# Performance work log

Measured on AMD Instinct MI355X. Metric: run time of the kernel, lower is better.

## Reference

```python
import jax, jax.numpy as jnp
import numpy as np

K = 15  # dynamic kernel size (out conv emits 15*15=225 channels)


def conv3x3(x, w, b):
    # x: [B,C,H,W], w: [O,I,3,3] (OIHW), 'SAME' padding, stride 1
    y = jax.lax.conv_general_dilated(
        x, w, window_strides=(1, 1), padding='SAME',
        dimension_numbers=('NCHW', 'OIHW', 'NCHW'))
    return y + b[None, :, None, None]


def res_block(x, wa, ba, wb, bb):
    # ResidualBlock_noBN: x + conv(relu(conv(x)))
    return x + conv3x3(jax.nn.relu(conv3x3(x, wa, ba)), wb, bb)


def setup_inputs() -> dict:
    key = jax.random.key(0)
    ks = jax.random.split(key, 12)
    nf = 64

    def w(k, o, i):
        return jax.random.normal(k, (o, i, 3, 3), jnp.float32) * 0.05

    return {
        'data_with_est': jax.random.normal(ks[0], (4, 6, 256, 256), jnp.float32),
        'data': jax.random.normal(ks[1], (4, 3, 256, 256), jnp.float32),
        'w_first': w(ks[2], nf, 6), 'b_first': jnp.zeros((nf,), jnp.float32),
        'w1a': w(ks[3], nf, nf), 'b1a': jnp.zeros((nf,), jnp.float32),
        'w1b': w(ks[4], nf, nf), 'b1b': jnp.zeros((nf,), jnp.float32),
        'w2a': w(ks[5], nf, nf), 'b2a': jnp.zeros((nf,), jnp.float32),
        'w2b': w(ks[6], nf, nf), 'b2b': jnp.zeros((nf,), jnp.float32),
        'w3a': w(ks[7], nf, nf), 'b3a': jnp.zeros((nf,), jnp.float32),
        'w3b': w(ks[8], nf, nf), 'b3b': jnp.zeros((nf,), jnp.float32),
        'w_out': w(ks[9], K * K, nf), 'b_out': jnp.zeros((K * K,), jnp.float32),
    }


def kernel_conv(frames, core):
    # frames: [B,3,H,W]; core: [B,225,H,W]
    B, C, H, W = frames.shape
    # per-pixel softmax over the 225 kernel taps of |core| (N=1, color=1 in original view)
    weights = jax.nn.softmax(jnp.abs(core), axis=1)  # [B, K*K, H, W]
    p = K // 2
    pad = jnp.pad(frames, ((0, 0), (0, 0), (p, p), (p, p)))
    shifts = jnp.arange(K)

    def win(i, j):  # shifted window, matches frame_pad[..., i:i+H, j:j+W]
        return jax.lax.dynamic_slice(pad, (0, 0, i, j), (B, C, H, W))

    # [K, K, B, C, H, W]; flattened index i*K+j matches torch stacking order
    patches = jax.vmap(lambda i: jax.vmap(lambda j: win(i, j))(shifts))(shifts)
    patches = patches.reshape(K * K, B, C, H, W)
    pred = jnp.einsum('bkhw,kbchw->bchw', weights, patches)  # sum over taps
    return pred


def reference(data_with_est, data,
              w_first, b_first,
              w1a, b1a, w1b, b1b,
              w2a, b2a, w2b, b2b,
              w3a, b3a, w3b, b3b,
              w_out, b_out):
    x = conv3x3(data_with_est, w_first, b_first)
    x = res_block(x, w1a, b1a, w1b, b1b)
    x = res_block(x, w2a, b2a, w2b, b2b)
    x = res_block(x, w3a, b3a, w3b, b3b)
    core = conv3x3(x, w_out, b_out)  # [B,225,H,W]
    pred = kernel_conv(data, core)   # [B,3,H,W]
    # original returns [frames, pred]
    return (data, pred)
```

## Files before the change

### kernel.cpp

```cpp
#include <hip/hip_runtime.h>

#define HW 256
#define PW 258
#define PP (PW * PW)
#define NPIX (HW * HW)

using short8 = __attribute__((ext_vector_type(8))) short;
using short4v = __attribute__((ext_vector_type(4))) short;
using f32x4 = __attribute__((ext_vector_type(4))) float;
using h4 = __attribute__((ext_vector_type(4))) _Float16;

#define GLD_LDS(g, l)                                                  \
  __builtin_amdgcn_global_load_lds(                                    \
      (const __attribute__((address_space(1))) void*)(g),              \
      (__attribute__((address_space(3))) void*)(l), 16, 0, 0)

static __device__ __forceinline__ ushort f2bf(float f) {
  unsigned u = __float_as_uint(f);
  unsigned r = (u + 0x7FFFu + ((u >> 16) & 1u)) >> 16;
  return (ushort)r;
}
static __device__ __forceinline__ float bf2f(ushort u) {
  return __uint_as_float(((unsigned)u) << 16);
}

__global__ void prep_pack_k(const float* __restrict__ din,
                            ushort* __restrict__ xp, ushort* __restrict__ x,
                            ushort* __restrict__ y,
                            const float4* __restrict__ data4,
                            float4* __restrict__ out4) {
  int blk = blockIdx.x, tid = threadIdx.x;
  if (blk < 1024) {
    int i = blk * 256 + tid;
    int b = i >> 16;
    int px = i & 65535;
    int yy = px >> 8, xx = px & 255;
    short8 v;
#pragma unroll
    for (int z = 0; z < 8; ++z) v[z] = 0;
#pragma unroll
    for (int ic = 0; ic < 6; ++ic)
      v[ic] = (short)f2bf(din[(b * 6 + ic) * NPIX + px]);
    *(short8*)&xp[((size_t)b * PP + (size_t)(yy + 1) * PW + (xx + 1)) * 8] = v;
  } else if (blk < 1041) {
    int i = (blk - 1024) * 256 + tid;
    if (i >= 4 * 1028) return;
    int b = i / 1028;
    int h = i - b * 1028;
    int py, px;
    if (h < 258) { py = 0; px = h; }
    else if (h < 516) { py = 257; px = h - 258; }
    else if (h < 772) { py = h - 516 + 1; px = 0; }
    else { py = h - 772 + 1; px = 257; }
    size_t p = (size_t)b * PP + (size_t)py * PW + px;
    short8 z;
#pragma unroll
    for (int k = 0; k < 8; ++k) z[k] = 0;
#pragma unroll
    for (int c8 = 0; c8 < 8; ++c8) {
      *(short8*)&x[p * 64 + c8 * 8] = z;
      *(short8*)&y[p * 64 + c8 * 8] = z;
    }
    *(short8*)&xp[p * 8] = z;
  } else {
    int i = (blk - 1041) * 256 + tid;
    if (i < 196608) out4[i] = data4[i];
  }
}

struct W8 { const float* w[8]; };

static __device__ __forceinline__ void pack_one(const float* __restrict__ w,
                                                ushort* __restrict__ wf, int OC,
                                                int CIN, int CPAD, int i,
                                                int total) {
  if (i >= total) return;
  int j = i & 7;
  int lane = (i >> 3) & 63;
  int rest = i >> 9;
  int NG = total >> 9;
  (void)NG;
  int NGr = (OC > 64) ? 16 : 4;
  int g = rest % NGr;
  int ks = rest / NGr;
  int oc = g * 16 + (lane & 15);
  int k = ks * 32 + (lane >> 4) * 8 + j;
  int t = k / CPAD;
  int ic = k - t * CPAD;
  float v = 0.f;
  if (oc < OC && t < 9 && ic < CIN) v = w[(oc * CIN + ic) * 9 + t];
  wf[i] = f2bf(v);
}

__global__ void prep_w_k(W8 ws, ushort* __restrict__ base) {
  int blk = blockIdx.x, tid = threadIdx.x;
  if (blk < 24) {
    pack_one(ws.w[0], base, 64, 6, 8, blk * 256 + tid, 6144);
  } else if (blk < 888) {
    int seg = (blk - 24) / 144;
    int i = ((blk - 24) - seg * 144) * 256 + tid;
    pack_one(ws.w[1 + seg], base + 6144 + seg * 36864, 64, 64, 64, i, 36864);
  } else {
    int i = (blk - 888) * 256 + tid;
    pack_one(ws.w[7], base + 227328, 225, 64, 64, i, 147456);
  }
}

template <int C, int KS, bool RELU, bool RESID>
__global__ __launch_bounds__(256, 2) void conv_mfma_k(
    const ushort* __restrict__ in, const ushort* __restrict__ wf,
    const float* __restrict__ bias, const ushort* __restrict__ resid,
    ushort* __restrict__ out) {
  constexpr int CV = C / 8;
  constexpr int SROW = 66 * CV;
  constexpr int TOT = 6 * SROW;
  constexpr int LSLOT = ((TOT + 63) / 64) * 64;
  constexpr int W = (KS > 4) ? 4 : KS;
  __shared__ __align__(16) ushort xs[LSLOT * 8];

  const int tid = threadIdx.x;
  const int wave = tid >> 6, lane = tid & 63;
  const int quad = lane >> 4, l15 = lane & 15;
  const int x0 = blockIdx.x * 64, y0 = blockIdx.y * 4, b = blockIdx.z;
  const ushort* inb = in + (size_t)b * PP * C;
  const ushort* wfl = wf + (size_t)lane * 8;

  for (int s0 = wave * 64; s0 < TOT; s0 += 256) {
    int s = s0 + lane;
    int row, col, chunk;
    if (C == 64) {
      row = s / SROW;
      int r = s - row * SROW;
      col = r >> 3;
      chunk = (r & 7) ^ (col & 7);
    } else {
      row = s / 66;
      col = s - row * 66;
      chunk = 0;
    }
    GLD_LDS(inb + ((size_t)(y0 + row) * PW + (x0 + col)) * C + chunk * 8,
            &xs[(size_t)s0 * 8]);
  }

  short8 Wa[4][W];
  auto loadA = [&](int slot, int ks) {
#pragma unroll
    for (int mt = 0; mt < 4; ++mt)
      Wa[mt][slot] = *(const short8*)&wfl[(size_t)(ks * 4 + mt) * 512];
  };
#pragma unroll
  for (int ks = 0; ks < W; ++ks) loadA(ks, ks);

  __syncthreads();

  f32x4 acc[4][4];
#pragma unroll
  for (int mt = 0; mt < 4; ++mt)
#pragma unroll
    for (int nt = 0; nt < 4; ++nt)
#pragma unroll
      for (int r = 0; r < 4; ++r) acc[mt][nt][r] = 0.f;

  auto loadB = [&](short8* B, int ks) {
    int t, chunk;
    if (C == 64) {
      t = ks >> 1;
      chunk = ((ks & 1) << 2) + quad;
    } else {
      t = ks * 4 + quad;
      if (t > 8) t = 8;
      chunk = 0;
    }
    int dy = t / 3, dx = t - (t / 3) * 3;
#pragma unroll
    for (int nt = 0; nt < 4; ++nt) {
      int c = nt * 16 + l15 + dx;
      int slot = (C == 64)
                     ? ((wave + dy) * SROW + c * 8 + (chunk ^ (c & 7)))
                     : ((wave + dy) * 66 + c);
      B[nt] = *(const short8*)&xs[(size_t)slot * 8];
    }
  };

  short8 Bbuf[2][4];
  loadB(Bbuf[0], 0);
#pragma unroll
  for (int ks = 0; ks < KS; ++ks) {
    if (ks + 1 < KS) loadB(Bbuf[(ks + 1) & 1], ks + 1);
    const int slot = ks % W;
#pragma unroll
    for (int nt = 0; nt < 4; ++nt)
#pragma unroll
      for (int mt = 0; mt < 4; ++mt)
        acc[mt][nt] = __builtin_amdgcn_mfma_f32_16x16x32_bf16(
            Wa[mt][slot], Bbuf[ks & 1][nt], acc[mt][nt], 0, 0, 0);
    if (ks + W < KS) loadA(slot, ks + W);
  }

  const int yw = y0 + wave;
#pragma unroll
  for (int mt = 0; mt < 4; ++mt) {
    const float4 bb = *(const float4*)&bias[mt * 16 + quad * 4];
#pragma unroll
    for (int nt = 0; nt < 4; ++nt) {
      int px = x0 + nt * 16 + l15;
      size_t base = ((size_t)b * PP + (size_t)(yw + 1) * PW + (px + 1)) * 64 +
                    mt * 16 + quad * 4;
      float v0 = acc[mt][nt][0] + bb.x;
      float v1 = acc[mt][nt][1] + bb.y;
      float v2 = acc[mt][nt][2] + bb.z;
      float v3 = acc[mt][nt][3] + bb.w;
      if (RELU) {
        v0 = fmaxf(v0, 0.f); v1 = fmaxf(v1, 0.f);
        v2 = fmaxf(v2, 0.f); v3 = fmaxf(v3, 0.f);
      }
      if (RESID) {
        short4v rv = *(const short4v*)&resid[base];
        v0 += bf2f((ushort)rv[0]); v1 += bf2f((ushort)rv[1]);
        v2 += bf2f((ushort)rv[2]); v3 += bf2f((ushort)rv[3]);
      }
      short4v o;
      o[0] = (short)f2bf(v0); o[1] = (short)f2bf(v1);
      o[2] = (short)f2bf(v2); o[3] = (short)f2bf(v3);
      *(short4v*)&out[base] = o;
    }
  }
}

__global__ __launch_bounds__(256, 2) void out_kc_k(
    const ushort* __restrict__ x, const ushort* __restrict__ wf,
    const float* __restrict__ b_out, const float* __restrict__ data,
    float* __restrict__ pred) {
  __shared__ __align__(16) char uni[64 * 264 * 2];
  __shared__ __align__(16) _Float16 dshT[3 * 80 * 20];
  __shared__ float bsh[256];
  ushort* xs = (ushort*)uni;
  _Float16* coreSh = (_Float16*)uni;

  const int tid = threadIdx.x;
  const int wave = tid >> 6, lane = tid & 63;
  const int quad = lane >> 4, l15 = lane & 15;
  const int x0 = blockIdx.x * 64, y = blockIdx.y, b = blockIdx.z;
  const ushort* wfl = wf + (size_t)lane * 8;

  for (int s0 = wave * 64; s0 < 3 * 528; s0 += 256) {
    int s = s0 + lane;
    int row = s / 528;
    int r = s - row * 528;
    int col = r >> 3;
    int chunk = (r & 7) ^ (col & 7);
    const ushort* g = x + ((size_t)b * PP + (size_t)(y + row) * PW +
                           (x0 + col)) * 64 + chunk * 8;
    GLD_LDS(g, &xs[(size_t)s0 * 8]);
  }
  bsh[tid] = (tid < 225) ? b_out[tid] : 0.f;
  for (int i = tid; i < 3 * 16 * 78; i += 256) {
    int ch = i / 1248;
    int rem = i - ch * 1248;
    int r = rem / 78;
    int col = rem - r * 78;
    int gy = y - 7 + r, gx = x0 - 7 + col;
    float v = 0.f;
    if ((unsigned)gy < (unsigned)HW && (unsigned)gx < (unsigned)HW)
      v = data[((b * 3 + ch) << 16) + (gy << 8) + gx];
    dshT[(ch * 80 + col) * 20 + r] = (_Float16)v;
  }

  short8 Wa[4][4];
  auto loadA = [&](int slot, int ks) {
#pragma unroll
    for (int mt = 0; mt < 4; ++mt)
      Wa[mt][slot] =
          *(const short8*)&wfl[(size_t)((ks * 16 + wave * 4 + mt)) * 512];
  };
#pragma unroll
  for (int ks = 0; ks < 4; ++ks) loadA(ks, ks);

  __syncthreads();

  f32x4 acc[4][4];
#pragma unroll
  for (int mt = 0; mt < 4; ++mt)
#pragma unroll
    for (int nt = 0; nt < 4; ++nt)
#pragma unroll
      for (int r = 0; r < 4; ++r) acc[mt][nt][r] = 0.f;

  auto loadB = [&](short8* B, int ks) {
    int t = ks >> 1;
    int dy = t / 3, dx = t - (t / 3) * 3;
    int chunk = ((ks & 1) << 2) + quad;
#pragma unroll
    for (int nt = 0; nt < 4; ++nt) {
      int c = nt * 16 + l15 + dx;
      int slot = dy * 528 + c * 8 + (chunk ^ (c & 7));
      B[nt] = *(const short8*)&xs[(size_t)slot * 8];
    }
  };

  short8 Bbuf[2][4];
  loadB(Bbuf[0], 0);
#pragma unroll
  for (int ks = 0; ks < 18; ++ks) {
    if (ks + 1 < 18) loadB(Bbuf[(ks + 1) & 1], ks + 1);
    const int slot = ks % 4;
#pragma unroll
    for (int nt = 0; nt < 4; ++nt)
#pragma unroll
      for (int mt = 0; mt < 4; ++mt)
        acc[mt][nt] = __builtin_amdgcn_mfma_f32_16x16x32_bf16(
            Wa[mt][slot], Bbuf[ks & 1][nt], acc[mt][nt], 0, 0, 0);
    if (ks + 4 < 18) loadA(slot, ks + 4);
  }
  __syncthreads();

#pragma unroll
  for (int mt = 0; mt < 4; ++mt) {
    int c0 = wave * 64 + mt * 16 + quad * 4;
#pragma unroll
    for (int nt = 0; nt < 4; ++nt) {
      int px = nt * 16 + l15;
      h4 hv;
#pragma unroll
      for (int r = 0; r < 4; ++r) {
        int c = c0 + r;
        float a = acc[mt][nt][r] + bsh[c];
        a = (c < 225) ? fabsf(a) : -1e4f;
        hv[r] = (_Float16)a;
      }
      *(h4*)&coreSh[px * 264 + c0] = hv;
    }
  }
  __syncthreads();

  const int px = wave * 16 + l15;
  const int q = quad;
  h4 vals4[15];
#pragma unroll
  for (int k = 0; k < 15; ++k)
    vals4[k] = *(h4*)&coreSh[px * 264 + q * 60 + k * 4];

  float m = 0.f;
#pragma unroll
  for (int k = 0; k < 15; ++k)
#pragma unroll
    for (int z = 0; z < 4; ++z) m = fmaxf(m, (float)vals4[k][z]);
  m = fmaxf(m, __shfl_xor(m, 16));
  m = fmaxf(m, __shfl_xor(m, 32));

  float e[60];
  float l = 0.f;
#pragma unroll
  for (int k = 0; k < 15; ++k)
#pragma unroll
    for (int z = 0; z < 4; ++z) {
      float t = __expf((float)vals4[k][z] - m);
      e[k * 4 + z] = t;
      l += t;
    }

  float p0 = 0.f, p1 = 0.f, p2 = 0.f;
#pragma unroll
  for (int dj = 0; dj < 15; ++dj) {
    h4 d0 = *(h4*)&dshT[(0 * 80 + px + dj) * 20 + 4 * q];
    h4 d1 = *(h4*)&dshT[(1 * 80 + px + dj) * 20 + 4 * q];
    h4 d2 = *(h4*)&dshT[(2 * 80 + px + dj) * 20 + 4 * q];
#pragma unroll
    for (int rr = 0; rr < 4; ++rr) {
      float ev = e[rr * 15 + dj];
      p0 += ev * (float)d0[rr];
      p1 += ev * (float)d1[rr];
      p2 += ev * (float)d2[rr];
    }
  }
  l += __shfl_xor(l, 16);  l += __shfl_xor(l, 32);
  p0 += __shfl_xor(p0, 16); p0 += __shfl_xor(p0, 32);
  p1 += __shfl_xor(p1, 16); p1 += __shfl_xor(p1, 32);
  p2 += __shfl_xor(p2, 16); p2 += __shfl_xor(p2, 32);

  if (q == 0) {
    float inv = 1.f / l;
    int pix = (y << 8) + x0 + px;
    pred[((b * 3 + 0) << 16) + pix] = p0 * inv;
    pred[((b * 3 + 1) << 16) + pix] = p1 * inv;
    pred[((b * 3 + 2) << 16) + pix] = p2 * inv;
  }
}

extern "C" void kernel_launch(void* const* d_in, const int* in_sizes, int n_in,
                              void* d_out, int out_size, void* d_ws,
                              size_t ws_size, hipStream_t stream) {
  const float* data_with_est = (const float*)d_in[0];
  const float* data = (const float*)d_in[1];
  const float* b_first = (const float*)d_in[3];
  const float* ba[3] = {(const float*)d_in[5], (const float*)d_in[9],
                        (const float*)d_in[13]};
  const float* bb[3] = {(const float*)d_in[7], (const float*)d_in[11],
                        (const float*)d_in[15]};
  const float* b_out = (const float*)d_in[17];

  float* out = (float*)d_out;
  float* pred = out + 4 * 3 * NPIX;

  ushort* x = (ushort*)d_ws;
  ushort* y = x + (size_t)4 * PP * 64;
  ushort* xp = y + (size_t)4 * PP * 64;
  ushort* Wb = xp + (size_t)4 * PP * 8;
  ushort* Wp1 = Wb;
  ushort* Wpr = Wb + 6144;
  ushort* Wpo = Wb + 227328;

  prep_pack_k<<<1809, 256, 0, stream>>>(data_with_est, xp, x, y,
                                        (const float4*)data, (float4*)out);
  W8 ws;
  ws.w[0] = (const float*)d_in[2];
  ws.w[1] = (const float*)d_in[4];  ws.w[2] = (const float*)d_in[6];
  ws.w[3] = (const float*)d_in[8];  ws.w[4] = (const float*)d_in[10];
  ws.w[5] = (const float*)d_in[12]; ws.w[6] = (const float*)d_in[14];
  ws.w[7] = (const float*)d_in[16];
  prep_w_k<<<1464, 256, 0, stream>>>(ws, Wb);

  dim3 cgrid(4, 64, 4), cblk(256);
  conv_mfma_k<8, 3, false, false>
      <<<cgrid, cblk, 0, stream>>>(xp, Wp1, b_first, nullptr, x);
  for (int i = 0; i < 3; ++i) {
    conv_mfma_k<64, 18, true, false><<<cgrid, cblk, 0, stream>>>(
        x, Wpr + (2 * i) * 36864, ba[i], nullptr, y);
    conv_mfma_k<64, 18, false, true><<<cgrid, cblk, 0, stream>>>(
        y, Wpr + (2 * i + 1) * 36864, bb[i], x, x);
  }
  out_kc_k<<<dim3(4, HW, 4), 256, 0, stream>>>(x, Wpo, b_out, data, pred);
}
```

Measured before the change: 443.1 us.

## Stage conv weights in LDS and use chunk-major activation layout

The conv kernel now copies the whole packed weight block into LDS with async global-to-LDS loads instead of streaming weight fragments from global memory into registers. The activation tile layout changes from an XOR-swizzled pixel-major layout to a chunk-major layout, in both the conv and output kernels. The MFMA loop gains a three-deep register pipeline for both A and B operands. For C=64 the launch bounds drop to one block per SM to fit the larger LDS footprint, which reduces occupancy. The unswizzled layout may also add LDS bank conflicts.

```diff
diff --git a/kernel.cpp b/kernel.cpp
--- a/kernel.cpp
+++ b/kernel.cpp
@@ -78,8 +78,6 @@
   int j = i & 7;
   int lane = (i >> 3) & 63;
   int rest = i >> 9;
-  int NG = total >> 9;
-  (void)NG;
   int NGr = (OC > 64) ? 16 : 4;
   int g = rest % NGr;
   int ks = rest / NGr;
@@ -107,60 +105,51 @@
 }
 
 template <int C, int KS, bool RELU, bool RESID>
-__global__ __launch_bounds__(256, 2) void conv_mfma_k(
+__global__ __launch_bounds__(256, (C == 8) ? 2 : 1) void conv_mfma_k(
     const ushort* __restrict__ in, const ushort* __restrict__ wf,
     const float* __restrict__ bias, const ushort* __restrict__ resid,
     ushort* __restrict__ out) {
   constexpr int CV = C / 8;
-  constexpr int SROW = 66 * CV;
-  constexpr int TOT = 6 * SROW;
-  constexpr int LSLOT = ((TOT + 63) / 64) * 64;
-  constexpr int W = (KS > 4) ? 4 : KS;
-  __shared__ __align__(16) ushort xs[LSLOT * 8];
+  constexpr int XSLOT = CV * 6 * 66;
+  constexpr int WSLOT = KS * 4 * 64;
+  __shared__ __align__(16) ushort wLds[WSLOT * 8];
+  __shared__ __align__(16) ushort xs[XSLOT * 8];
 
   const int tid = threadIdx.x;
   const int wave = tid >> 6, lane = tid & 63;
   const int quad = lane >> 4, l15 = lane & 15;
   const int x0 = blockIdx.x * 64, y0 = blockIdx.y * 4, b = blockIdx.z;
   const ushort* inb = in + (size_t)b * PP * C;
-  const ushort* wfl = wf + (size_t)lane * 8;
-
-  for (int s0 = wave * 64; s0 < TOT; s0 += 256) {
+
+  for (int s0 = wave * 64; s0 < WSLOT; s0 += 256)
+    GLD_LDS(wf + (size_t)(s0 + lane) * 8, &wLds[(size_t)s0 * 8]);
+
+  for (int s0 = wave * 64; s0 < XSLOT; s0 += 256) {
     int s = s0 + lane;
-    int row, col, chunk;
-    if (C == 64) {
-      row = s / SROW;
-      int r = s - row * SROW;
-      col = r >> 3;
-      chunk = (r & 7) ^ (col & 7);
-    } else {
-      row = s / 66;
-      col = s - row * 66;
-      chunk = 0;
-    }
-    GLD_LDS(inb + ((size_t)(y0 + row) * PW + (x0 + col)) * C + chunk * 8,
-            &xs[(size_t)s0 * 8]);
-  }
-
-  short8 Wa[4][W];
-  auto loadA = [&](int slot, int ks) {
+    if (s < XSLOT) {
+      int chunk = (CV == 1) ? 0 : (s / 396);
+      int rem = (CV == 1) ? s : (s - chunk * 396);
+      int row = rem / 66;
+      int col = rem - row * 66;
+      GLD_LDS(inb + ((size_t)(y0 + row) * PW + (x0 + col)) * C + chunk * 8,
+              &xs[(size_t)s0 * 8]);
+    }
+  }
+  __syncthreads();
+
+  f32x4 acc[4][4];
+#pragma unroll
+  for (int mt = 0; mt < 4; ++mt)
+#pragma unroll
+    for (int nt = 0; nt < 4; ++nt)
+#pragma unroll
+      for (int r = 0; r < 4; ++r) acc[mt][nt][r] = 0.f;
+
+  auto loadA = [&](short8* A, int ks) {
 #pragma unroll
     for (int mt = 0; mt < 4; ++mt)
-      Wa[mt][slot] = *(const short8*)&wfl[(size_t)(ks * 4 + mt) * 512];
+      A[mt] = *(const short8*)&wLds[((ks * 4 + mt) * 64 + lane) * 8];
   };
-#pragma unroll
-  for (int ks = 0; ks < W; ++ks) loadA(ks, ks);
-
-  __syncthreads();
-
-  f32x4 acc[4][4];
-#pragma unroll
-  for (int mt = 0; mt < 4; ++mt)
-#pragma unroll
-    for (int nt = 0; nt < 4; ++nt)
-#pragma unroll
-      for (int r = 0; r < 4; ++r) acc[mt][nt][r] = 0.f;
-
   auto loadB = [&](short8* B, int ks) {
     int t, chunk;
     if (C == 64) {
@@ -174,27 +163,27 @@
     int dy = t / 3, dx = t - (t / 3) * 3;
 #pragma unroll
     for (int nt = 0; nt < 4; ++nt) {
-      int c = nt * 16 + l15 + dx;
-      int slot = (C == 64)
-                     ? ((wave + dy) * SROW + c * 8 + (chunk ^ (c & 7)))
-                     : ((wave + dy) * 66 + c);
+      int col = nt * 16 + l15 + dx;
+      int slot = (chunk * 6 + wave + dy) * 66 + col;
       B[nt] = *(const short8*)&xs[(size_t)slot * 8];
     }
   };
 
-  short8 Bbuf[2][4];
-  loadB(Bbuf[0], 0);
+  short8 A[3][4], B[3][4];
+  loadA(A[0], 0); loadB(B[0], 0);
+  if (KS > 1) { loadA(A[1], 1); loadB(B[1], 1); }
 #pragma unroll
   for (int ks = 0; ks < KS; ++ks) {
-    if (ks + 1 < KS) loadB(Bbuf[(ks + 1) & 1], ks + 1);
-    const int slot = ks % W;
+    if (ks + 2 < KS) {
+      loadA(A[(ks + 2) % 3], ks + 2);
+      loadB(B[(ks + 2) % 3], ks + 2);
+    }
 #pragma unroll
     for (int nt = 0; nt < 4; ++nt)
 #pragma unroll
       for (int mt = 0; mt < 4; ++mt)
         acc[mt][nt] = __builtin_amdgcn_mfma_f32_16x16x32_bf16(
-            Wa[mt][slot], Bbuf[ks & 1][nt], acc[mt][nt], 0, 0, 0);
-    if (ks + W < KS) loadA(slot, ks + W);
+            A[ks % 3][mt], B[ks % 3][nt], acc[mt][nt], 0, 0, 0);
   }
 
   const int yw = y0 + wave;
@@ -243,15 +232,17 @@
   const int x0 = blockIdx.x * 64, y = blockIdx.y, b = blockIdx.z;
   const ushort* wfl = wf + (size_t)lane * 8;
 
-  for (int s0 = wave * 64; s0 < 3 * 528; s0 += 256) {
+  for (int s0 = wave * 64; s0 < 1584; s0 += 256) {
     int s = s0 + lane;
-    int row = s / 528;
-    int r = s - row * 528;
-    int col = r >> 3;
-    int chunk = (r & 7) ^ (col & 7);
-    const ushort* g = x + ((size_t)b * PP + (size_t)(y + row) * PW +
-                           (x0 + col)) * 64 + chunk * 8;
-    GLD_LDS(g, &xs[(size_t)s0 * 8]);
+    if (s < 1584) {
+      int chunk = s / 198;
+      int rem = s - chunk * 198;
+      int row = rem / 66;
+      int col = rem - row * 66;
+      GLD_LDS(x + ((size_t)b * PP + (size_t)(y + row) * PW + (x0 + col)) * 64 +
+                  chunk * 8,
+              &xs[(size_t)s0 * 8]);
+    }
   }
   bsh[tid] = (tid < 225) ? b_out[tid] : 0.f;
   for (int i = tid; i < 3 * 16 * 78; i += 256) {
@@ -292,8 +283,8 @@
     int chunk = ((ks & 1) << 2) + quad;
 #pragma unroll
     for (int nt = 0; nt < 4; ++nt) {
-      int c = nt * 16 + l15 + dx;
-      int slot = dy * 528 + c * 8 + (chunk ^ (c & 7));
+      int col = nt * 16 + l15 + dx;
+      int slot = (chunk * 3 + dy) * 66 + col;
       B[nt] = *(const short8*)&xs[(size_t)slot * 8];
     }
   };
```

Result: slower. 467.1 us (+5.4%).
